# Optimization experiments

Hardware: AMD Instinct MI355X
Metric: run time of the kernel (lower is better)

The kernel has to match this reference:

```python
import jax, jax.numpy as jnp
import numpy as np

D_MODEL = 512
N_HEAD = 8


def setup_inputs() -> dict:
    key = jax.random.key(0)
    ks = jax.random.split(key, 9)
    s = 1.0 / np.sqrt(D_MODEL)
    inp = {
        "x": jax.random.normal(ks[0], (2, 4096, D_MODEL), dtype=jnp.float32),
        "wq": jax.random.uniform(ks[1], (D_MODEL, D_MODEL), jnp.float32, -s, s),
        "bq": jax.random.uniform(ks[2], (D_MODEL,), jnp.float32, -s, s),
        "wk": jax.random.uniform(ks[3], (D_MODEL, D_MODEL), jnp.float32, -s, s),
        "bk": jax.random.uniform(ks[4], (D_MODEL,), jnp.float32, -s, s),
        "wv": jax.random.uniform(ks[5], (D_MODEL, D_MODEL), jnp.float32, -s, s),
        "bv": jax.random.uniform(ks[6], (D_MODEL,), jnp.float32, -s, s),
        "wo": jax.random.uniform(ks[7], (D_MODEL, D_MODEL), jnp.float32, -s, s),
        "bo": jax.random.uniform(ks[8], (D_MODEL,), jnp.float32, -s, s),
    }
    return inp


def reference(x, wq, bq, wk, bk, wv, bv, wo, bo):
    B, S, D = x.shape
    H = N_HEAD
    Dh = D // H

    def split_heads(t):  # [B,S,D] -> [B,H,S,Dh]
        return t.reshape(B, S, H, Dh).transpose(0, 2, 1, 3)

    q = split_heads(x @ wq.T + bq)
    k = split_heads(x @ wk.T + bk)
    v = split_heads(x @ wv.T + bv)

    # explicit (unfused) attention, matching the torch module
    score = jnp.einsum("bhsd,bhtd->bhst", q, k) / jnp.sqrt(jnp.float32(Dh))
    attn = jax.nn.softmax(score, axis=-1)
    out = jnp.einsum("bhst,bhtd->bhsd", attn, v)  # [B,H,S,Dh]

    out = out.transpose(0, 2, 1, 3).reshape(B, S, D)
    return out @ wo.T + bo
```

## Files before the change

### kernel.cpp

```cpp
#include <hip/hip_runtime.h>
#include <math.h>

#define S_LEN 4096
#define DMODEL 512
#define NHEAD 8
#define E_ELEMS ((size_t)8192 * 512)
#define QSCALE 0.18033688f

typedef __attribute__((ext_vector_type(8))) short bf16x8;
typedef __attribute__((ext_vector_type(4))) float f32x4;
typedef __attribute__((ext_vector_type(16))) float f32x16;
typedef unsigned short u16;
typedef unsigned int u32;

__device__ __forceinline__ u16 f2bf(float f) {
    u32 u = __float_as_uint(f);
    u += 0x7FFFu + ((u >> 16) & 1u);
    return (u16)(u >> 16);
}
__device__ __forceinline__ float bf2f(u16 h) {
    return __uint_as_float((u32)h << 16);
}

#define MFMA16(a, b, c) __builtin_amdgcn_mfma_f32_16x16x32_bf16((a), (b), (c), 0, 0, 0)
#define MFMA32(a, b, c) __builtin_amdgcn_mfma_f32_32x32x16_bf16((a), (b), (c), 0, 0, 0)

__global__ __launch_bounds__(256) void cvt_x(const float* __restrict__ in,
                                             u16* __restrict__ out, int n4) {
    const int i = blockIdx.x * 256 + threadIdx.x;
    if (i >= n4) return;
    const float4 v = ((const float4*)in)[i];
    uint2 hp;
    hp.x = (u32)f2bf(v.x) | ((u32)f2bf(v.y) << 16);
    hp.y = (u32)f2bf(v.z) | ((u32)f2bf(v.w) << 16);
    ((uint2*)out)[i] = hp;
}

__global__ __launch_bounds__(256) void cvt_w(
    const float* __restrict__ wq, const float* __restrict__ wk,
    const float* __restrict__ wv, const float* __restrict__ wo,
    u16* __restrict__ oq, u16* __restrict__ ok,
    u16* __restrict__ ov, u16* __restrict__ oo) {
    const int i = blockIdx.x * 256 + threadIdx.x;
    {
        const float4 v = ((const float4*)wq)[i];
        uint2 hp;
        hp.x = (u32)f2bf(v.x * QSCALE) | ((u32)f2bf(v.y * QSCALE) << 16);
        hp.y = (u32)f2bf(v.z * QSCALE) | ((u32)f2bf(v.w * QSCALE) << 16);
        ((uint2*)oq)[i] = hp;
    }
    {
        const float4 v = ((const float4*)wk)[i];
        uint2 hp;
        hp.x = (u32)f2bf(v.x) | ((u32)f2bf(v.y) << 16);
        hp.y = (u32)f2bf(v.z) | ((u32)f2bf(v.w) << 16);
        ((uint2*)ok)[i] = hp;
    }
    {
        const float4 v = ((const float4*)wv)[i];
        uint2 hp;
        hp.x = (u32)f2bf(v.x) | ((u32)f2bf(v.y) << 16);
        hp.y = (u32)f2bf(v.z) | ((u32)f2bf(v.w) << 16);
        ((uint2*)ov)[i] = hp;
    }
    {
        const float4 v = ((const float4*)wo)[i];
        uint2 hp;
        hp.x = (u32)f2bf(v.x) | ((u32)f2bf(v.y) << 16);
        hp.y = (u32)f2bf(v.z) | ((u32)f2bf(v.w) << 16);
        ((uint2*)oo)[i] = hp;
    }
}

template<int MODE>
__global__ __launch_bounds__(256) void proj2_kernel(
    const u16* __restrict__ Abf,
    const u16* __restrict__ W0, const float* __restrict__ Bi0,
    const u16* __restrict__ W1, const float* __restrict__ Bi1,
    u16* __restrict__ Qo, u16* __restrict__ Ko, float* __restrict__ Out)
{
    __shared__ __align__(16) u16 sm[16384];
    u16* As = sm;
    u16* Bs = sm + 8192;

    const int tid = threadIdx.x;
    const int w = tid >> 6, l = tid & 63, g = (l >> 4), c = l & 15;
    const int wr = w >> 1, wc = w & 1;
    const int bm = blockIdx.x * 128;
    const int n0 = blockIdx.y * 128;
    const int z = (MODE == 0) ? blockIdx.z : 0;
    const u16* W   = z ? W1 : W0;
    const float* Bi = z ? Bi1 : Bi0;
    const float bsc = (MODE == 0 && z == 0) ? QSCALE : 1.0f;

    const int sr = l >> 3;
    const int slot = l & 7;

    f32x4 acc[4][4];
    #pragma unroll
    for (int i = 0; i < 4; ++i)
        #pragma unroll
        for (int j = 0; j < 4; ++j) acc[i][j] = (f32x4){0.f, 0.f, 0.f, 0.f};

    #pragma unroll 1
    for (int kt = 0; kt < 8; ++kt) {
        const int k0 = kt * 64;
        __syncthreads();
        #pragma unroll
        for (int i = 0; i < 4; ++i) {
            const int row = i * 32 + w * 8 + sr;
            const int scol = (slot ^ (row & 7)) * 8;
            __builtin_amdgcn_global_load_lds(
                Abf + (size_t)(bm + row) * DMODEL + k0 + scol,
                As + (i * 32 + w * 8) * 64, 16, 0, 0);
            __builtin_amdgcn_global_load_lds(
                W + (size_t)(n0 + row) * DMODEL + k0 + scol,
                Bs + (i * 32 + w * 8) * 64, 16, 0, 0);
        }
        __syncthreads();

        #pragma unroll
        for (int kc = 0; kc < 2; ++kc) {
            bf16x8 a[4], b[4];
            #pragma unroll
            for (int mf = 0; mf < 4; ++mf) {
                const int ra = wr * 64 + mf * 16 + c;
                a[mf] = *(const bf16x8*)(As + ra * 64 + (((kc * 4 + g) ^ (ra & 7)) * 8));
            }
            #pragma unroll
            for (int nf = 0; nf < 4; ++nf) {
                const int rb = wc * 64 + nf * 16 + c;
                b[nf] = *(const bf16x8*)(Bs + rb * 64 + (((kc * 4 + g) ^ (rb & 7)) * 8));
            }
            #pragma unroll
            for (int mf = 0; mf < 4; ++mf)
                #pragma unroll
                for (int nf = 0; nf < 4; ++nf)
                    acc[mf][nf] = MFMA16(a[mf], b[nf], acc[mf][nf]);
        }
    }

    #pragma unroll
    for (int mf = 0; mf < 4; ++mf)
        #pragma unroll
        for (int nf = 0; nf < 4; ++nf) {
            const int n = n0 + wc * 64 + nf * 16 + c;
            const float bias = Bi[n] * bsc;
            #pragma unroll
            for (int r = 0; r < 4; ++r) {
                const int m = bm + wr * 64 + mf * 16 + 4 * g + r;
                const float v = acc[mf][nf][r] + bias;
                if (MODE == 1) {
                    Out[(size_t)m * DMODEL + n] = v;
                } else {
                    const int b = m >> 12, s = m & (S_LEN - 1);
                    const int hh = n >> 6, dd = n & 63;
                    const size_t o = ((size_t)((b * NHEAD + hh) * S_LEN + s)) * 64 + dd;
                    if (z == 0) Qo[o] = f2bf(v);
                    else        Ko[o] = f2bf(v);
                }
            }
        }
}

__global__ __launch_bounds__(256) void proj_v_kernel(
    const u16* __restrict__ Abf, const u16* __restrict__ Wv,
    const float* __restrict__ Bv, u16* __restrict__ Vt)
{
    __shared__ __align__(16) u16 sm[18432];
    u16* Ah = sm;
    u16* Bh = sm + 9216;

    const int tid = threadIdx.x;
    const int w = tid >> 6, lane = tid & 63, g = lane >> 4, c = lane & 15;
    const int bm = blockIdx.x * 128;
    const int n0 = blockIdx.y * 64;

    f32x4 acc[2][4];
    #pragma unroll
    for (int a = 0; a < 2; ++a)
        #pragma unroll
        for (int b = 0; b < 4; ++b) acc[a][b] = (f32x4){0.f, 0.f, 0.f, 0.f};

    #pragma unroll 1
    for (int kt = 0; kt < 8; ++kt) {
        const int k0 = kt * 64;
        __syncthreads();
        #pragma unroll
        for (int i = 0; i < 4; ++i) {
            const int slot = i * 256 + tid;
            const int r = slot >> 3, c8 = slot & 7;
            *(uint4*)(Ah + r * 72 + c8 * 8) =
                *(const uint4*)(Abf + (size_t)(bm + r) * DMODEL + k0 + c8 * 8);
        }
        #pragma unroll
        for (int i = 0; i < 2; ++i) {
            const int slot = i * 256 + tid;
            const int r = slot >> 3, c8 = slot & 7;
            *(uint4*)(Bh + r * 72 + c8 * 8) =
                *(const uint4*)(Wv + (size_t)(n0 + r) * DMODEL + k0 + c8 * 8);
        }
        __syncthreads();

        #pragma unroll
        for (int kc = 0; kc < 2; ++kc) {
            bf16x8 a[2], b[4];
            #pragma unroll
            for (int mf = 0; mf < 2; ++mf)
                a[mf] = *(const bf16x8*)(Ah + (w * 32 + mf * 16 + c) * 72 + kc * 32 + g * 8);
            #pragma unroll
            for (int nf = 0; nf < 4; ++nf)
                b[nf] = *(const bf16x8*)(Bh + (nf * 16 + c) * 72 + kc * 32 + g * 8);
            #pragma unroll
            for (int mf = 0; mf < 2; ++mf)
                #pragma unroll
                for (int nf = 0; nf < 4; ++nf)
                    acc[mf][nf] = MFMA16(a[mf], b[nf], acc[mf][nf]);
        }
    }

    __syncthreads();
    float* scr = (float*)sm;
    #pragma unroll
    for (int mf = 0; mf < 2; ++mf)
        #pragma unroll
        for (int nf = 0; nf < 4; ++nf) {
            const float bias = Bv[n0 + nf * 16 + c];
            #pragma unroll
            for (int r = 0; r < 4; ++r)
                scr[(w * 32 + mf * 16 + 4 * g + r) * 72 + nf * 16 + c] =
                    acc[mf][nf][r] + bias;
        }
    __syncthreads();
    const int d = tid & 63, sb = tid >> 6;
    const int b = bm >> 12, h = n0 >> 6;
    const size_t obase =
        ((size_t)((b * NHEAD + h) * 64 + d)) * S_LEN + (bm & (S_LEN - 1)) + sb * 32;
    u16 th[32];
    #pragma unroll
    for (int j = 0; j < 32; ++j)
        th[j] = f2bf(scr[(sb * 32 + j) * 72 + d]);
    #pragma unroll
    for (int q = 0; q < 4; ++q)
        *(uint4*)(Vt + obase + q * 8) = *(const uint4*)&th[q * 8];
}

__global__ __launch_bounds__(256, 4) void attn_kernel(
    const u16* __restrict__ Qb, const u16* __restrict__ Kb,
    const u16* __restrict__ Vt, u16* __restrict__ OpB, float* __restrict__ Lp)
{
    __shared__ __align__(16) u16 sm[16384];

    const int tid = threadIdx.x;
    const int w = tid >> 6, l = tid & 63;
    const int r0 = l & 31, hi = l >> 5;

    const int f = blockIdx.x;
    const int wg = (f & 7) * 256 + (f >> 3);
    const int bh = wg >> 7, kvq = (wg >> 5) & 3, qb = wg & 31;
    const int b = bh >> 3, h = bh & 7;

    const size_t hoff = (size_t)bh * S_LEN * 64;
    const int qw = qb * 128 + w * 32;
    const int kv0 = kvq * 1024;

    bf16x8 qf[4];
    #pragma unroll
    for (int kc = 0; kc < 4; ++kc)
        qf[kc] = *(const bf16x8*)(Qb + hoff + (size_t)(qw + r0) * 64 + kc * 16 + hi * 8);

    const int rbase = r0 * 64;
    int soff[4];
    #pragma unroll
    for (int j = 0; j < 4; ++j) soff[j] = ((2 * j + hi) ^ (r0 & 7)) * 8;

    const int srow0 = w * 16 + (l >> 3);
    const int slot  = l & 7;
    const int srow1 = srow0 + 8;
    const u16* srcK0 = Kb + hoff + (size_t)(kv0 + srow0) * 64 + ((slot ^ (srow0 & 7)) * 8);
    const u16* srcK1 = Kb + hoff + (size_t)(kv0 + srow1) * 64 + ((slot ^ (srow1 & 7)) * 8);
    const u16* srcV0 = Vt + ((size_t)bh * 64 + srow0) * S_LEN + kv0 + ((slot ^ (srow0 & 7)) * 8);
    const u16* srcV1 = Vt + ((size_t)bh * 64 + srow1) * S_LEN + kv0 + ((slot ^ (srow1 & 7)) * 8);

#define STAGE(bufb, t) do {                                                        \
        u16* kb_ = sm + (bufb) * 8192 + w * 1024;                                  \
        u16* vb_ = kb_ + 4096;                                                     \
        __builtin_amdgcn_global_load_lds(srcK0 + (size_t)(t) * 4096, kb_,       16, 0, 0); \
        __builtin_amdgcn_global_load_lds(srcK1 + (size_t)(t) * 4096, kb_ + 512, 16, 0, 0); \
        __builtin_amdgcn_global_load_lds(srcV0 + (size_t)(t) * 64,   vb_,       16, 0, 0); \
        __builtin_amdgcn_global_load_lds(srcV1 + (size_t)(t) * 64,   vb_ + 512, 16, 0, 0); \
    } while (0)

    f32x16 o0 = {0.f,0.f,0.f,0.f,0.f,0.f,0.f,0.f,0.f,0.f,0.f,0.f,0.f,0.f,0.f,0.f};
    f32x16 o1 = {0.f,0.f,0.f,0.f,0.f,0.f,0.f,0.f,0.f,0.f,0.f,0.f,0.f,0.f,0.f,0.f};
    f32x16 lacc = {0.f,0.f,0.f,0.f,0.f,0.f,0.f,0.f,0.f,0.f,0.f,0.f,0.f,0.f,0.f,0.f};

    STAGE(0, 0);
    __syncthreads();
    int buf = 0;

    #pragma unroll 1
    for (int t = 0; t < 16; ++t) {
        if (t + 1 < 16) STAGE(buf ^ 1, t + 1);

        const u16* Kb_s = sm + buf * 8192;
        const u16* Vb_s = Kb_s + 4096;

        f32x16 s0 = {0.f,0.f,0.f,0.f,0.f,0.f,0.f,0.f,0.f,0.f,0.f,0.f,0.f,0.f,0.f,0.f};
        f32x16 s1 = {0.f,0.f,0.f,0.f,0.f,0.f,0.f,0.f,0.f,0.f,0.f,0.f,0.f,0.f,0.f,0.f};
        __builtin_amdgcn_s_setprio(1);
        #pragma unroll
        for (int kc = 0; kc < 4; ++kc) {
            const bf16x8 k0 = *(const bf16x8*)(Kb_s + rbase + soff[kc]);
            const bf16x8 k1 = *(const bf16x8*)(Kb_s + 2048 + rbase + soff[kc]);
            s0 = MFMA32(k0, qf[kc], s0);
            s1 = MFMA32(k1, qf[kc], s1);
        }
        __builtin_amdgcn_s_setprio(0);

        bf16x8 pa[4];
        #pragma unroll
        for (int kvf = 0; kvf < 2; ++kvf) {
            f32x16 pex;
            #pragma unroll
            for (int r = 0; r < 16; ++r)
                pex[r] = __builtin_amdgcn_exp2f(kvf ? s1[r] : s0[r]);
            lacc += pex;
            #pragma unroll
            for (int hf = 0; hf < 2; ++hf) {
                const int rb = hf * 8;
                u32 x0, y0, x1, y1;
                asm("v_cvt_pk_bf16_f32 %0, %1, %2" : "=v"(x0) : "v"(pex[rb+0]), "v"(pex[rb+1]));
                asm("v_cvt_pk_bf16_f32 %0, %1, %2" : "=v"(y0) : "v"(pex[rb+4]), "v"(pex[rb+5]));
                asm("v_cvt_pk_bf16_f32 %0, %1, %2" : "=v"(x1) : "v"(pex[rb+2]), "v"(pex[rb+3]));
                asm("v_cvt_pk_bf16_f32 %0, %1, %2" : "=v"(y1) : "v"(pex[rb+6]), "v"(pex[rb+7]));
                asm volatile("v_permlane32_swap_b32 %0, %1" : "+v"(x0), "+v"(y0));
                asm volatile("v_permlane32_swap_b32 %0, %1" : "+v"(x1), "+v"(y1));
                union { u32 u[4]; bf16x8 v; } P;
                P.u[0] = x0; P.u[1] = x1; P.u[2] = y0; P.u[3] = y1;
                pa[kvf * 2 + hf] = P.v;
            }
        }

        __builtin_amdgcn_s_setprio(1);
        #pragma unroll
        for (int kvc = 0; kvc < 4; ++kvc) {
            const bf16x8 v0 = *(const bf16x8*)(Vb_s + rbase + soff[kvc]);
            const bf16x8 v1 = *(const bf16x8*)(Vb_s + 2048 + rbase + soff[kvc]);
            o0 = MFMA32(pa[kvc], v0, o0);
            o1 = MFMA32(pa[kvc], v1, o1);
        }
        __builtin_amdgcn_s_setprio(0);

        __syncthreads();
        buf ^= 1;
    }
#undef STAGE

    float lsum = 0.f;
    #pragma unroll
    for (int r = 0; r < 16; ++r) lsum += lacc[r];
    lsum += __shfl_xor(lsum, 32);
    if (hi == 0)
        Lp[((size_t)kvq * 16 + bh) * S_LEN + qw + r0] = lsum;

    u16* Ob = OpB + (size_t)kvq * E_ELEMS + (size_t)b * S_LEN * DMODEL;
    #pragma unroll
    for (int df = 0; df < 2; ++df) {
        #pragma unroll
        for (int r = 0; r < 16; ++r) {
            const float ov = df ? o1[r] : o0[r];
            const int q = (r & 3) + 8 * (r >> 2) + 4 * hi;
            Ob[(size_t)(qw + q) * DMODEL + h * 64 + df * 32 + r0] = f2bf(ov);
        }
    }
}

__global__ __launch_bounds__(256) void combine_kernel(
    const u16* __restrict__ Op, const float* __restrict__ Lp,
    u16* __restrict__ A)
{
    const int i = blockIdx.x * 256 + threadIdx.x;
    const int m = i >> 6;
    const int col = (i & 63) * 8;
    const int b = m >> 12, s = m & (S_LEN - 1), h = col >> 6;

    float lt = 0.f;
    #pragma unroll
    for (int kq = 0; kq < 4; ++kq)
        lt += Lp[((size_t)kq * 16 + b * 8 + h) * S_LEN + s];
    const float inv = 1.0f / lt;

    float acc[8] = {};
    #pragma unroll
    for (int kq = 0; kq < 4; ++kq) {
        const uint4 v = *(const uint4*)(Op + (size_t)kq * E_ELEMS + (size_t)m * DMODEL + col);
        const u16* p = (const u16*)&v;
        #pragma unroll
        for (int j = 0; j < 8; ++j) acc[j] += bf2f(p[j]);
    }
    u16 r[8];
    #pragma unroll
    for (int j = 0; j < 8; ++j) r[j] = f2bf(acc[j] * inv);
    *(uint4*)(A + (size_t)m * DMODEL + col) = *(const uint4*)r;
}

extern "C" void kernel_launch(void* const* d_in, const int* in_sizes, int n_in,
                              void* d_out, int out_size, void* d_ws, size_t ws_size,
                              hipStream_t stream)
{
    const float* x  = (const float*)d_in[0];
    const float* wq = (const float*)d_in[1];
    const float* bq = (const float*)d_in[2];
    const float* wk = (const float*)d_in[3];
    const float* bk = (const float*)d_in[4];
    const float* wv = (const float*)d_in[5];
    const float* bv = (const float*)d_in[6];
    const float* wo = (const float*)d_in[7];
    const float* bo = (const float*)d_in[8];

    u16* ws = (u16*)d_ws;
    const size_t E = E_ELEMS;
    u16* xbf  = ws;
    u16* Qbf  = ws + E;
    u16* Kbf  = ws + 2 * E;
    u16* Vtbf = ws + 3 * E;
    u16* wqbf = ws + 4 * E;
    u16* wkbf = wqbf + DMODEL * DMODEL;
    u16* wvbf = wkbf + DMODEL * DMODEL;
    u16* wobf = wvbf + DMODEL * DMODEL;
    u16* OpB  = wobf + DMODEL * DMODEL;
    float* Lp = (float*)(OpB + 4 * E);

    cvt_x<<<dim3(4096), 256, 0, stream>>>(x, xbf, (int)(E / 4));
    cvt_w<<<dim3(256), 256, 0, stream>>>(wq, wk, wv, wo, wqbf, wkbf, wvbf, wobf);

    proj2_kernel<0><<<dim3(64, 4, 2), 256, 0, stream>>>(
        xbf, wqbf, bq, wkbf, bk, Qbf, Kbf, nullptr);

    proj_v_kernel<<<dim3(64, 8), 256, 0, stream>>>(xbf, wvbf, bv, Vtbf);

    attn_kernel<<<dim3(2048), 256, 0, stream>>>(Qbf, Kbf, Vtbf, OpB, Lp);

    combine_kernel<<<dim3(2048), 256, 0, stream>>>(OpB, Lp, xbf);

    proj2_kernel<1><<<dim3(64, 4), 256, 0, stream>>>(
        xbf, wobf, bo, nullptr, nullptr, nullptr, nullptr, (float*)d_out);
}
```

Before: 148.8 us.

## Double per-wave query rows in attention and halve the KV split

Each wave now processes 64 query rows instead of 32, reusing every K and V fragment loaded from shared memory for two MFMA chains. The KV dimension is split into 2 parts instead of 4, so the grid shrinks from 2048 to 512 blocks, and the combine kernel reads half as many partial outputs and sums. This is meant to cut LDS traffic per FLOP and the partial-output write/read traffic. In exchange it raises register pressure (launch bounds drop to 2 blocks per SM) and leaves fewer blocks for the GPU's many compute units, which may hurt latency hiding and load balance.

```diff
diff --git a/kernel.cpp b/kernel.cpp
--- a/kernel.cpp
+++ b/kernel.cpp
@@ -245,7 +245,7 @@
         *(uint4*)(Vt + obase + q * 8) = *(const uint4*)&th[q * 8];
 }
 
-__global__ __launch_bounds__(256, 4) void attn_kernel(
+__global__ __launch_bounds__(256, 2) void attn_kernel(
     const u16* __restrict__ Qb, const u16* __restrict__ Kb,
     const u16* __restrict__ Vt, u16* __restrict__ OpB, float* __restrict__ Lp)
 {
@@ -256,18 +256,21 @@
     const int r0 = l & 31, hi = l >> 5;
 
     const int f = blockIdx.x;
-    const int wg = (f & 7) * 256 + (f >> 3);
-    const int bh = wg >> 7, kvq = (wg >> 5) & 3, qb = wg & 31;
+    const int wg = (f & 7) * 64 + (f >> 3);
+    const int bh = wg >> 5, kvh = (wg >> 4) & 1, qb = wg & 15;
     const int b = bh >> 3, h = bh & 7;
 
     const size_t hoff = (size_t)bh * S_LEN * 64;
-    const int qw = qb * 128 + w * 32;
-    const int kv0 = kvq * 1024;
-
-    bf16x8 qf[4];
-    #pragma unroll
-    for (int kc = 0; kc < 4; ++kc)
-        qf[kc] = *(const bf16x8*)(Qb + hoff + (size_t)(qw + r0) * 64 + kc * 16 + hi * 8);
+    const int qw = qb * 256 + w * 64;
+    const int kv0 = kvh * 2048;
+
+    bf16x8 qf[2][4];
+    #pragma unroll
+    for (int qfi = 0; qfi < 2; ++qfi)
+        #pragma unroll
+        for (int kc = 0; kc < 4; ++kc)
+            qf[qfi][kc] = *(const bf16x8*)(Qb + hoff +
+                (size_t)(qw + qfi * 32 + r0) * 64 + kc * 16 + hi * 8);
 
     const int rbase = r0 * 64;
     int soff[4];
@@ -291,54 +294,62 @@
         __builtin_amdgcn_global_load_lds(srcV1 + (size_t)(t) * 64,   vb_ + 512, 16, 0, 0); \
     } while (0)
 
-    f32x16 o0 = {0.f,0.f,0.f,0.f,0.f,0.f,0.f,0.f,0.f,0.f,0.f,0.f,0.f,0.f,0.f,0.f};
-    f32x16 o1 = {0.f,0.f,0.f,0.f,0.f,0.f,0.f,0.f,0.f,0.f,0.f,0.f,0.f,0.f,0.f,0.f};
-    f32x16 lacc = {0.f,0.f,0.f,0.f,0.f,0.f,0.f,0.f,0.f,0.f,0.f,0.f,0.f,0.f,0.f,0.f};
+#define ZERO16 {0.f,0.f,0.f,0.f,0.f,0.f,0.f,0.f,0.f,0.f,0.f,0.f,0.f,0.f,0.f,0.f}
+    f32x16 o00 = ZERO16, o01 = ZERO16, o10 = ZERO16, o11 = ZERO16;
+    f32x16 laccA = ZERO16, laccB = ZERO16;
 
     STAGE(0, 0);
     __syncthreads();
     int buf = 0;
 
     #pragma unroll 1
-    for (int t = 0; t < 16; ++t) {
-        if (t + 1 < 16) STAGE(buf ^ 1, t + 1);
+    for (int t = 0; t < 32; ++t) {
+        if (t + 1 < 32) STAGE(buf ^ 1, t + 1);
 
         const u16* Kb_s = sm + buf * 8192;
         const u16* Vb_s = Kb_s + 4096;
 
-        f32x16 s0 = {0.f,0.f,0.f,0.f,0.f,0.f,0.f,0.f,0.f,0.f,0.f,0.f,0.f,0.f,0.f,0.f};
-        f32x16 s1 = {0.f,0.f,0.f,0.f,0.f,0.f,0.f,0.f,0.f,0.f,0.f,0.f,0.f,0.f,0.f,0.f};
-        __builtin_amdgcn_s_setprio(1);
-        #pragma unroll
-        for (int kc = 0; kc < 4; ++kc) {
-            const bf16x8 k0 = *(const bf16x8*)(Kb_s + rbase + soff[kc]);
-            const bf16x8 k1 = *(const bf16x8*)(Kb_s + 2048 + rbase + soff[kc]);
-            s0 = MFMA32(k0, qf[kc], s0);
-            s1 = MFMA32(k1, qf[kc], s1);
-        }
-        __builtin_amdgcn_s_setprio(0);
-
-        bf16x8 pa[4];
+        bf16x8 pa0[4], pa1[4];
         #pragma unroll
         for (int kvf = 0; kvf < 2; ++kvf) {
-            f32x16 pex;
-            #pragma unroll
-            for (int r = 0; r < 16; ++r)
-                pex[r] = __builtin_amdgcn_exp2f(kvf ? s1[r] : s0[r]);
-            lacc += pex;
+            f32x16 sA = ZERO16, sB = ZERO16;
+            __builtin_amdgcn_s_setprio(1);
+            #pragma unroll
+            for (int kc = 0; kc < 4; ++kc) {
+                const bf16x8 k = *(const bf16x8*)(Kb_s + kvf * 2048 + rbase + soff[kc]);
+                sA = MFMA32(k, qf[0][kc], sA);
+                sB = MFMA32(k, qf[1][kc], sB);
+            }
+            __builtin_amdgcn_s_setprio(0);
+            #pragma unroll
+            for (int r = 0; r < 16; ++r) {
+                sA[r] = __builtin_amdgcn_exp2f(sA[r]);
+                sB[r] = __builtin_amdgcn_exp2f(sB[r]);
+            }
+            laccA += sA;
+            laccB += sB;
             #pragma unroll
             for (int hf = 0; hf < 2; ++hf) {
                 const int rb = hf * 8;
                 u32 x0, y0, x1, y1;
-                asm("v_cvt_pk_bf16_f32 %0, %1, %2" : "=v"(x0) : "v"(pex[rb+0]), "v"(pex[rb+1]));
-                asm("v_cvt_pk_bf16_f32 %0, %1, %2" : "=v"(y0) : "v"(pex[rb+4]), "v"(pex[rb+5]));
-                asm("v_cvt_pk_bf16_f32 %0, %1, %2" : "=v"(x1) : "v"(pex[rb+2]), "v"(pex[rb+3]));
-                asm("v_cvt_pk_bf16_f32 %0, %1, %2" : "=v"(y1) : "v"(pex[rb+6]), "v"(pex[rb+7]));
+                asm("v_cvt_pk_bf16_f32 %0, %1, %2" : "=v"(x0) : "v"(sA[rb+0]), "v"(sA[rb+1]));
+                asm("v_cvt_pk_bf16_f32 %0, %1, %2" : "=v"(y0) : "v"(sA[rb+4]), "v"(sA[rb+5]));
+                asm("v_cvt_pk_bf16_f32 %0, %1, %2" : "=v"(x1) : "v"(sA[rb+2]), "v"(sA[rb+3]));
+                asm("v_cvt_pk_bf16_f32 %0, %1, %2" : "=v"(y1) : "v"(sA[rb+6]), "v"(sA[rb+7]));
                 asm volatile("v_permlane32_swap_b32 %0, %1" : "+v"(x0), "+v"(y0));
                 asm volatile("v_permlane32_swap_b32 %0, %1" : "+v"(x1), "+v"(y1));
-                union { u32 u[4]; bf16x8 v; } P;
-                P.u[0] = x0; P.u[1] = x1; P.u[2] = y0; P.u[3] = y1;
-                pa[kvf * 2 + hf] = P.v;
+                union { u32 u[4]; bf16x8 v; } PA;
+                PA.u[0] = x0; PA.u[1] = x1; PA.u[2] = y0; PA.u[3] = y1;
+                pa0[kvf * 2 + hf] = PA.v;
+                asm("v_cvt_pk_bf16_f32 %0, %1, %2" : "=v"(x0) : "v"(sB[rb+0]), "v"(sB[rb+1]));
+                asm("v_cvt_pk_bf16_f32 %0, %1, %2" : "=v"(y0) : "v"(sB[rb+4]), "v"(sB[rb+5]));
+                asm("v_cvt_pk_bf16_f32 %0, %1, %2" : "=v"(x1) : "v"(sB[rb+2]), "v"(sB[rb+3]));
+                asm("v_cvt_pk_bf16_f32 %0, %1, %2" : "=v"(y1) : "v"(sB[rb+6]), "v"(sB[rb+7]));
+                asm volatile("v_permlane32_swap_b32 %0, %1" : "+v"(x0), "+v"(y0));
+                asm volatile("v_permlane32_swap_b32 %0, %1" : "+v"(x1), "+v"(y1));
+                union { u32 u[4]; bf16x8 v; } PB;
+                PB.u[0] = x0; PB.u[1] = x1; PB.u[2] = y0; PB.u[3] = y1;
+                pa1[kvf * 2 + hf] = PB.v;
             }
         }
 
@@ -347,8 +358,10 @@
         for (int kvc = 0; kvc < 4; ++kvc) {
             const bf16x8 v0 = *(const bf16x8*)(Vb_s + rbase + soff[kvc]);
             const bf16x8 v1 = *(const bf16x8*)(Vb_s + 2048 + rbase + soff[kvc]);
-            o0 = MFMA32(pa[kvc], v0, o0);
-            o1 = MFMA32(pa[kvc], v1, o1);
+            o00 = MFMA32(pa0[kvc], v0, o00);
+            o01 = MFMA32(pa0[kvc], v1, o01);
+            o10 = MFMA32(pa1[kvc], v0, o10);
+            o11 = MFMA32(pa1[kvc], v1, o11);
         }
         __builtin_amdgcn_s_setprio(0);
 
@@ -357,23 +370,28 @@
     }
 #undef STAGE
 
-    float lsum = 0.f;
-    #pragma unroll
-    for (int r = 0; r < 16; ++r) lsum += lacc[r];
-    lsum += __shfl_xor(lsum, 32);
-    if (hi == 0)
-        Lp[((size_t)kvq * 16 + bh) * S_LEN + qw + r0] = lsum;
-
-    u16* Ob = OpB + (size_t)kvq * E_ELEMS + (size_t)b * S_LEN * DMODEL;
-    #pragma unroll
-    for (int df = 0; df < 2; ++df) {
-        #pragma unroll
-        for (int r = 0; r < 16; ++r) {
-            const float ov = df ? o1[r] : o0[r];
-            const int q = (r & 3) + 8 * (r >> 2) + 4 * hi;
-            Ob[(size_t)(qw + q) * DMODEL + h * 64 + df * 32 + r0] = f2bf(ov);
-        }
-    }
+    float l0 = 0.f, l1 = 0.f;
+    #pragma unroll
+    for (int r = 0; r < 16; ++r) { l0 += laccA[r]; l1 += laccB[r]; }
+    l0 += __shfl_xor(l0, 32);
+    l1 += __shfl_xor(l1, 32);
+    if (hi == 0) {
+        Lp[((size_t)kvh * 16 + bh) * S_LEN + qw + r0]      = l0;
+        Lp[((size_t)kvh * 16 + bh) * S_LEN + qw + 32 + r0] = l1;
+    }
+
+    u16* Ob = OpB + (size_t)kvh * E_ELEMS + (size_t)b * S_LEN * DMODEL;
+    #pragma unroll
+    for (int qfi = 0; qfi < 2; ++qfi)
+        #pragma unroll
+        for (int df = 0; df < 2; ++df) {
+            #pragma unroll
+            for (int r = 0; r < 16; ++r) {
+                const float ov = qfi ? (df ? o11[r] : o10[r]) : (df ? o01[r] : o00[r]);
+                const int q = qfi * 32 + (r & 3) + 8 * (r >> 2) + 4 * hi;
+                Ob[(size_t)(qw + q) * DMODEL + h * 64 + df * 32 + r0] = f2bf(ov);
+            }
+        }
 }
 
 __global__ __launch_bounds__(256) void combine_kernel(
@@ -384,16 +402,15 @@
     const int m = i >> 6;
     const int col = (i & 63) * 8;
     const int b = m >> 12, s = m & (S_LEN - 1), h = col >> 6;
-
-    float lt = 0.f;
-    #pragma unroll
-    for (int kq = 0; kq < 4; ++kq)
-        lt += Lp[((size_t)kq * 16 + b * 8 + h) * S_LEN + s];
+    const int bh = b * 8 + h;
+
+    const float lt = Lp[(size_t)bh * S_LEN + s] +
+                     Lp[((size_t)16 + bh) * S_LEN + s];
     const float inv = 1.0f / lt;
 
     float acc[8] = {};
     #pragma unroll
-    for (int kq = 0; kq < 4; ++kq) {
+    for (int kq = 0; kq < 2; ++kq) {
         const uint4 v = *(const uint4*)(Op + (size_t)kq * E_ELEMS + (size_t)m * DMODEL + col);
         const u16* p = (const u16*)&v;
         #pragma unroll
@@ -430,7 +447,7 @@
     u16* wvbf = wkbf + DMODEL * DMODEL;
     u16* wobf = wvbf + DMODEL * DMODEL;
     u16* OpB  = wobf + DMODEL * DMODEL;
-    float* Lp = (float*)(OpB + 4 * E);
+    float* Lp = (float*)(OpB + 2 * E);
 
     cvt_x<<<dim3(4096), 256, 0, stream>>>(x, xbf, (int)(E / 4));
     cvt_w<<<dim3(256), 256, 0, stream>>>(wq, wk, wv, wo, wqbf, wkbf, wvbf, wobf);
@@ -440,7 +457,7 @@
 
     proj_v_kernel<<<dim3(64, 8), 256, 0, stream>>>(xbf, wvbf, bv, Vtbf);
 
-    attn_kernel<<<dim3(2048), 256, 0, stream>>>(Qbf, Kbf, Vtbf, OpB, Lp);
+    attn_kernel<<<dim3(512), 256, 0, stream>>>(Qbf, Kbf, Vtbf, OpB, Lp);
 
     combine_kernel<<<dim3(2048), 256, 0, stream>>>(OpB, Lp, xbf);
 
```

New measurement: 134.4 us. -9.7%, faster.
